# Kernel optimization log

Measured on AMD Instinct MI355X. Metric: run time of the kernel, lower is better.

## Reference

```python
import jax, jax.numpy as jnp
import numpy as np

B, C, H, W = 8, 512, 32, 32
NUM_HEADS = 8
HEAD_DIM = C // NUM_HEADS


def setup_inputs() -> dict:
    key = jax.random.key(0)
    k1, k2, k3 = jax.random.split(key, 3)
    query = jax.random.normal(k1, (B, C, H, W), dtype=jnp.float32)
    key_value = jax.random.normal(k2, (B, C, H, W), dtype=jnp.float32)
    # Linear(dim, 3*dim): store as [C, 3C] so y = x @ W + b
    W_qkv = jax.random.normal(k3, (C, 3 * C), dtype=jnp.float32) * (C ** -0.5)
    b_qkv = jnp.zeros((3 * C,), dtype=jnp.float32)
    return {"query": query, "key_value": key_value, "W_qkv": W_qkv, "b_qkv": b_qkv}


def reference(query, key_value, W_qkv, b_qkv):
    Bb, Cc, Hh, Ww = query.shape
    seq = Hh * Ww
    scale = HEAD_DIM ** -0.5

    # [B, C, H, W] -> [B, S, C]
    q_seq = query.reshape(Bb, Cc, seq).transpose(0, 2, 1)
    kv_seq = key_value.reshape(Bb, Cc, seq).transpose(0, 2, 1)

    # Original calls full qkv_proj and slices; math == projecting with sliced weights.
    q = q_seq @ W_qkv[:, :Cc] + b_qkv[:Cc]
    k = kv_seq @ W_qkv[:, Cc:2 * Cc] + b_qkv[Cc:2 * Cc]
    v = kv_seq @ W_qkv[:, 2 * Cc:] + b_qkv[2 * Cc:]

    def heads(x):  # [B, S, C] -> [B, nH, S, hd]
        return x.reshape(Bb, seq, NUM_HEADS, HEAD_DIM).transpose(0, 2, 1, 3)

    q, k, v = heads(q), heads(k), heads(v)
    attn = jnp.einsum('bhqd,bhkd->bhqk', q, k) * scale
    attn = jax.nn.softmax(attn, axis=-1)  # dropout: identity in eval
    out = jnp.einsum('bhqk,bhkd->bhqd', attn, v)
    # [B, nH, S, hd] -> [B, S, C] -> [B, C, H, W]
    out = out.transpose(0, 2, 1, 3).reshape(Bb, seq, Cc)
    return out.transpose(0, 2, 1).reshape(Bb, Cc, Hh, Ww)
```

## Files before the change

### kernel.cpp

```cpp
#include <hip/hip_runtime.h>
#include <hip/hip_bf16.h>

using short4v = __attribute__((ext_vector_type(4))) short;
using short8  = __attribute__((ext_vector_type(8))) short;
using uint2v  = __attribute__((ext_vector_type(2))) unsigned int;
using f32x4   = __attribute__((ext_vector_type(4))) float;

static constexpr int CDIM = 512;
static constexpr float KSCALE = 0.125f * 1.44269504088896341f;

__device__ __forceinline__ short f2bf(float f) {
  unsigned u = __builtin_bit_cast(unsigned, f);
  u = (u + 0x7fffu + ((u >> 16) & 1u)) >> 16;
  return (short)(unsigned short)u;
}

#define GLOAD_LDS16(gp, lp)                                                              \
  __builtin_amdgcn_global_load_lds((const __attribute__((address_space(1))) void*)(gp),  \
                                   (__attribute__((address_space(3))) void*)(lp), 16, 0, 0)
#define MFMA16(a, b, c) __builtin_amdgcn_mfma_f32_16x16x32_bf16((a), (b), (c), 0, 0, 0)

#define LDS_FENCE()                        \
  do {                                     \
    asm volatile("" ::: "memory");         \
    __builtin_amdgcn_s_waitcnt(0xc07f);    \
    __builtin_amdgcn_sched_barrier(0);     \
  } while (0)

#define TILE_SYNC(N)                                          \
  do {                                                        \
    __builtin_amdgcn_sched_barrier(0);                        \
    asm volatile("s_waitcnt vmcnt(" #N ")" ::: "memory");     \
    __builtin_amdgcn_sched_barrier(0);                        \
    __builtin_amdgcn_s_barrier();                             \
    asm volatile("" ::: "memory");                            \
    __builtin_amdgcn_sched_barrier(0);                        \
  } while (0)

#define TILE_BAR()                                            \
  do {                                                        \
    __builtin_amdgcn_sched_barrier(0);                        \
    asm volatile("s_waitcnt lgkmcnt(0)" ::: "memory");        \
    __builtin_amdgcn_sched_barrier(0);                        \
    __builtin_amdgcn_s_barrier();                             \
    asm volatile("" ::: "memory");                            \
    __builtin_amdgcn_sched_barrier(0);                        \
  } while (0)

__global__ __launch_bounds__(256) void prep_transpose(const float* __restrict__ query,
                                                      const float* __restrict__ keyv,
                                                      const float* __restrict__ Wqkv,
                                                      short* __restrict__ Xq_t,
                                                      short* __restrict__ Xkv_t,
                                                      short* __restrict__ W_t) {
  __shared__ float tile[64 * 65];
  const int id = blockIdx.x;
  const float* s; short* d; int R, C, r0, c0;
  if (id < 2048) {
    const int which = id >> 10;
    int rem = id & 1023;
    const int b = rem >> 7; rem &= 127;
    R = 512; C = 1024;
    s = (which ? keyv : query) + (size_t)b * 512 * 1024;
    d = (which ? Xkv_t : Xq_t) + (size_t)b * 512 * 1024;
    r0 = (rem >> 4) * 64; c0 = (rem & 15) * 64;
  } else {
    const int rem = id - 2048;
    R = 512; C = 1536; s = Wqkv; d = W_t;
    r0 = (rem / 24) * 64; c0 = (rem % 24) * 64;
  }
  const int t  = threadIdx.x;
  const int rr = t >> 4;
  const int c4 = (t & 15) * 4;
#pragma unroll
  for (int i = 0; i < 4; ++i) {
    const int r = rr + i * 16;
    f32x4 v = *(const f32x4*)(s + (size_t)(r0 + r) * C + c0 + c4);
#pragma unroll
    for (int j = 0; j < 4; ++j) tile[(c4 + j) * 65 + r] = v[j];
  }
  __syncthreads();
  const int r8 = (t & 7) * 8;
#pragma unroll
  for (int i = 0; i < 2; ++i) {
    const int c = (t >> 3) + i * 32;
    short8 pk;
#pragma unroll
    for (int j = 0; j < 8; ++j) pk[j] = f2bf(tile[c * 65 + r8 + j]);
    *(short8*)(d + (size_t)(c0 + c) * R + r0 + r8) = pk;
  }
}

__global__ __launch_bounds__(256, 3) void qkv_gemm(const short* __restrict__ Xq,
                                                   const short* __restrict__ Xkv,
                                                   const short* __restrict__ Wt,
                                                   const float* __restrict__ bias,
                                                   short* __restrict__ Qg,
                                                   short* __restrict__ Kg,
                                                   short* __restrict__ Vt) {
  __shared__ short Asm[128 * 64];
  __shared__ short Bsm[128 * 64];
  __shared__ short epi[4 * 1152];
  const int id = blockIdx.x;
  const int qq = id >> 3;
  const int m_blk = ((id & 7) << 3) | (qq & 7);
  const int n_blk = qq >> 3;
  const int m0 = m_blk << 7;
  const int n0 = n_blk << 7;
  const short* A = (n0 < CDIM) ? Xq : Xkv;
  const int t = threadIdx.x;
  const int w = t >> 6, l = t & 63;
  const int wm = w & 1, wn = w >> 1;
  const int lc = l & 15, lr = l >> 4;

  f32x4 acc[4][4];
#pragma unroll
  for (int i = 0; i < 4; ++i)
#pragma unroll
    for (int j = 0; j < 4; ++j) acc[i][j] = (f32x4){0.f, 0.f, 0.f, 0.f};

  for (int kb = 0; kb < 8; ++kb) {
    const int k0 = kb * 64;
#pragma unroll
    for (int i = 0; i < 4; ++i) {
      const int Qi = (w * 4 + i) * 64 + l;
      const int row = Qi >> 3, u = Qi & 7;
      GLOAD_LDS16(A + (size_t)(m0 + row) * CDIM + k0 + ((u ^ (row & 7)) * 8), &Asm[Qi * 8]);
      GLOAD_LDS16(Wt + (size_t)(n0 + row) * CDIM + k0 + ((u ^ (row & 7)) * 8), &Bsm[Qi * 8]);
    }
    __syncthreads();
#pragma unroll
    for (int kc = 0; kc < 2; ++kc) {
      short8 af[4], bfr[4];
#pragma unroll
      for (int mt = 0; mt < 4; ++mt) {
        const int row = wm * 64 + mt * 16 + lc;
        af[mt] = *(const short8*)(&Asm[(row * 8 + ((kc * 4 + lr) ^ (row & 7))) * 8]);
      }
#pragma unroll
      for (int nt = 0; nt < 4; ++nt) {
        const int row = wn * 64 + nt * 16 + lc;
        bfr[nt] = *(const short8*)(&Bsm[(row * 8 + ((kc * 4 + lr) ^ (row & 7))) * 8]);
      }
#pragma unroll
      for (int mt = 0; mt < 4; ++mt)
#pragma unroll
        for (int nt = 0; nt < 4; ++nt)
          acc[mt][nt] = MFMA16(af[mt], bfr[nt], acc[mt][nt]);
    }
    __syncthreads();
  }

  const int M0 = m0 + wm * 64;
  const int bb = M0 >> 10, s0 = M0 & 1023;
  const int N0 = n0 + wn * 64;
  float bv[4];
#pragma unroll
  for (int nt = 0; nt < 4; ++nt) bv[nt] = bias[N0 + nt * 16 + lc];
  short* slab = epi + w * 1152;

  const int hg = N0 >> 6;
  const int part = hg >> 3, hh = hg & 7;
  if (part < 2) {
    const float osc = part ? 1.f : KSCALE;
    short* obase = (part ? Kg : Qg) + (size_t)(bb * 8 + hh) * 65536 + (size_t)s0 * 64;
#pragma unroll
    for (int mt = 0; mt < 4; ++mt) {
#pragma unroll
      for (int ntL = 0; ntL < 4; ++ntL)
#pragma unroll
        for (int r = 0; r < 4; ++r)
          slab[(lr * 4 + r) * 72 + ntL * 16 + lc] =
              f2bf((acc[mt][ntL][r] + bv[ntL]) * osc);
      LDS_FENCE();
#pragma unroll
      for (int i = 0; i < 2; ++i) {
        const int slot = i * 64 + l;
        const int m_l = slot >> 3, n8 = (slot & 7) * 8;
        short8 vv = *(const short8*)(&slab[m_l * 72 + n8]);
        *(short8*)(obase + (size_t)(mt * 16 + m_l) * 64 + n8) = vv;
      }
      LDS_FENCE();
    }
  } else {
    short* vbase = Vt + (size_t)(bb * 8 + hh) * 65536;
#pragma unroll
    for (int ntL = 0; ntL < 4; ++ntL) {
#pragma unroll
      for (int mt = 0; mt < 4; ++mt)
#pragma unroll
        for (int r = 0; r < 4; ++r)
          slab[lc * 72 + mt * 16 + lr * 4 + r] = f2bf(acc[mt][ntL][r] + bv[ntL]);
      LDS_FENCE();
#pragma unroll
      for (int i = 0; i < 2; ++i) {
        const int slot = i * 64 + l;
        const int dloc = slot >> 3, ch = (slot & 7) * 8;
        short8 vv = *(const short8*)(&slab[dloc * 72 + ch]);
        *(short8*)(vbase + (size_t)(ntL * 16 + dloc) * 1024 + s0 + ch) = vv;
      }
      LDS_FENCE();
    }
  }
}

__global__ __launch_bounds__(256, 2) void flash_attn(const short* __restrict__ Qg,
                                                     const short* __restrict__ Kg,
                                                     const short* __restrict__ Vt,
                                                     float* __restrict__ out) {
  __shared__ alignas(16) short smem[25600];
  short* Ksm = smem;
  short* Vsm = smem + 8192;
  const int bh = blockIdx.x;
  const int b = bh >> 3, h = bh & 7;
  const int q0 = blockIdx.y * 128;
  const int t = threadIdx.x;
  const int w = t >> 6, l = t & 63;
  const int quad = l >> 4, l15 = l & 15;
  short* Pw = smem + 16384 + w * 2304;

  const short* Qbase = Qg + (size_t)bh * 65536;
  const short* Kbase = Kg + (size_t)bh * 65536;
  const short* Vbase = Vt + (size_t)bh * 65536;

  short8 bq[2][2];
#pragma unroll
  for (int qs = 0; qs < 2; ++qs) {
    const short* qrow = Qbase + (size_t)(q0 + qs * 64 + w * 16 + l15) * 64;
    bq[qs][0] = *(const short8*)(qrow + quad * 8);
    bq[qs][1] = *(const short8*)(qrow + 32 + quad * 8);
  }

  float lp[2] = {0.f, 0.f};
  f32x4 Oac[2][4];
#pragma unroll
  for (int qs = 0; qs < 2; ++qs)
#pragma unroll
    for (int dt = 0; dt < 4; ++dt) Oac[qs][dt] = (f32x4){0.f, 0.f, 0.f, 0.f};

  auto stage_tile = [&](int tile, int buf) {
    const int kk0 = tile * 64;
    short* Kd = Ksm + buf * 4096;
    short* Vd = Vsm + buf * 4096;
#pragma unroll
    for (int i = 0; i < 2; ++i) {
      const int Qi = (w * 2 + i) * 64 + l;
      const int sr = Qi >> 3, u = Qi & 7;
      GLOAD_LDS16(Kbase + (size_t)(kk0 + sr) * 64 + (u ^ (sr & 7)) * 8, &Kd[Qi * 8]);
      GLOAD_LDS16(Vbase + (size_t)sr * 1024 + kk0 + (u ^ (sr & 7)) * 8, &Vd[Qi * 8]);
    }
  };

  stage_tile(0, 0);
  for (int tt = 0; tt < 16; ++tt) {
    const int buf = tt & 1;
    if (tt < 15) {
      stage_tile(tt + 1, buf ^ 1);
      TILE_SYNC(4);
    } else {
      TILE_SYNC(0);
    }

    const short* Kh = Ksm + buf * 4096;
    const short* Vh = Vsm + buf * 4096;
    short8 kf[2][4];
#pragma unroll
    for (int c = 0; c < 2; ++c)
#pragma unroll
      for (int nt = 0; nt < 4; ++nt) {
        const int srow = nt * 16 + l15;
        kf[c][nt] = *(const short8*)(&Kh[(srow * 8 + ((c * 4 + quad) ^ (srow & 7))) * 8]);
      }

#pragma unroll
    for (int qs = 0; qs < 2; ++qs) {
      f32x4 st[4];
      __builtin_amdgcn_s_setprio(1);
#pragma unroll
      for (int nt = 0; nt < 4; ++nt) {
        st[nt] = (f32x4){0.f, 0.f, 0.f, 0.f};
#pragma unroll
        for (int c = 0; c < 2; ++c) st[nt] = MFMA16(kf[c][nt], bq[qs][c], st[nt]);
      }
      __builtin_amdgcn_s_setprio(0);
      short* Ps = Pw + qs * 1152;
#pragma unroll
      for (int nt = 0; nt < 4; ++nt) {
        float p0 = __builtin_amdgcn_exp2f(st[nt][0]);
        float p1 = __builtin_amdgcn_exp2f(st[nt][1]);
        float p2 = __builtin_amdgcn_exp2f(st[nt][2]);
        float p3 = __builtin_amdgcn_exp2f(st[nt][3]);
        lp[qs] += (p0 + p1) + (p2 + p3);
        unsigned pk0, pk1;
        asm("v_cvt_pk_bf16_f32 %0, %1, %2" : "=v"(pk0) : "v"(p0), "v"(p1));
        asm("v_cvt_pk_bf16_f32 %0, %1, %2" : "=v"(pk1) : "v"(p2), "v"(p3));
        uint2v pk; pk[0] = pk0; pk[1] = pk1;
        *(short4v*)(&Ps[l15 * 72 + (nt * 4 + quad) * 4]) = __builtin_bit_cast(short4v, pk);
      }
    }
    LDS_FENCE();

    __builtin_amdgcn_s_setprio(1);
#pragma unroll
    for (int c = 0; c < 2; ++c) {
      short8 pb0 = *(const short8*)(&Pw[l15 * 72 + (c * 8 + quad * 2) * 4]);
      short8 pb1 = *(const short8*)(&Pw[1152 + l15 * 72 + (c * 8 + quad * 2) * 4]);
#pragma unroll
      for (int dt = 0; dt < 4; ++dt) {
        const int drow = dt * 16 + l15;
        short8 vf = *(const short8*)(&Vh[(drow * 8 + ((c * 4 + quad) ^ (drow & 7))) * 8]);
        Oac[0][dt] = MFMA16(vf, pb0, Oac[0][dt]);
        Oac[1][dt] = MFMA16(vf, pb1, Oac[1][dt]);
      }
    }
    __builtin_amdgcn_s_setprio(0);
    TILE_BAR();
  }

#pragma unroll
  for (int qs = 0; qs < 2; ++qs) {
    float lv = lp[qs];
    lv += __shfl_xor(lv, 16, 64);
    lv += __shfl_xor(lv, 32, 64);
    const float rinv = 1.f / lv;
    float* ob = out + ((size_t)(b * 512 + h * 64)) * 1024 + q0 + qs * 64 + w * 16 + l15;
#pragma unroll
    for (int dt = 0; dt < 4; ++dt)
#pragma unroll
      for (int r = 0; r < 4; ++r)
        ob[(size_t)(dt * 16 + quad * 4 + r) * 1024] = Oac[qs][dt][r] * rinv;
  }
}

extern "C" void kernel_launch(void* const* d_in, const int* in_sizes, int n_in,
                              void* d_out, int out_size, void* d_ws, size_t ws_size,
                              hipStream_t stream) {
  const float* query = (const float*)d_in[0];
  const float* keyv  = (const float*)d_in[1];
  const float* Wqkv  = (const float*)d_in[2];
  const float* bqkv  = (const float*)d_in[3];
  float* out = (float*)d_out;
  short* ws  = (short*)d_ws;

  short* Xq_t  = ws;
  short* Xkv_t = ws + 4194304;
  short* W_t   = ws + 8388608;
  short* Qg    = ws + 9175040;
  short* Kg    = ws + 13369344;
  short* Vt    = ws + 17563648;

  prep_transpose<<<dim3(2240), 256, 0, stream>>>(query, keyv, Wqkv, Xq_t, Xkv_t, W_t);
  qkv_gemm<<<dim3(768), 256, 0, stream>>>(Xq_t, Xkv_t, W_t, bqkv, Qg, Kg, Vt);
  flash_attn<<<dim3(64, 8, 1), 256, 0, stream>>>(Qg, Kg, Vt, out);
}
```

Before: 127.2 us.

## Halve flash-attention query tile to 64 rows and swizzle P buffer in LDS

Each attention block now processes 64 query rows instead of 128, doubling the grid to 1024 blocks and raising the launch bound to 4 blocks per CU. Register and LDS use per block shrink, which allows more concurrent waves to hide latency. The per-wave P scratch drops its padded 72-stride layout for a 64-stride XOR-swizzled layout to avoid bank conflicts with less LDS. In exchange, each K/V tile is loaded from global memory twice as often relative to the compute done on it.

```diff
diff --git a/kernel.cpp b/kernel.cpp
--- a/kernel.cpp
+++ b/kernel.cpp
@@ -204,39 +204,36 @@
   }
 }
 
-__global__ __launch_bounds__(256, 2) void flash_attn(const short* __restrict__ Qg,
+__global__ __launch_bounds__(256, 4) void flash_attn(const short* __restrict__ Qg,
                                                      const short* __restrict__ Kg,
                                                      const short* __restrict__ Vt,
                                                      float* __restrict__ out) {
-  __shared__ alignas(16) short smem[25600];
+  __shared__ alignas(16) short smem[20480];
   short* Ksm = smem;
   short* Vsm = smem + 8192;
   const int bh = blockIdx.x;
   const int b = bh >> 3, h = bh & 7;
-  const int q0 = blockIdx.y * 128;
+  const int q0 = blockIdx.y * 64;
   const int t = threadIdx.x;
   const int w = t >> 6, l = t & 63;
   const int quad = l >> 4, l15 = l & 15;
-  short* Pw = smem + 16384 + w * 2304;
+  short* Pw = smem + 16384 + w * 1024;
 
   const short* Qbase = Qg + (size_t)bh * 65536;
   const short* Kbase = Kg + (size_t)bh * 65536;
   const short* Vbase = Vt + (size_t)bh * 65536;
 
-  short8 bq[2][2];
-#pragma unroll
-  for (int qs = 0; qs < 2; ++qs) {
-    const short* qrow = Qbase + (size_t)(q0 + qs * 64 + w * 16 + l15) * 64;
-    bq[qs][0] = *(const short8*)(qrow + quad * 8);
-    bq[qs][1] = *(const short8*)(qrow + 32 + quad * 8);
-  }
-
-  float lp[2] = {0.f, 0.f};
-  f32x4 Oac[2][4];
-#pragma unroll
-  for (int qs = 0; qs < 2; ++qs)
-#pragma unroll
-    for (int dt = 0; dt < 4; ++dt) Oac[qs][dt] = (f32x4){0.f, 0.f, 0.f, 0.f};
+  short8 bq[2];
+  {
+    const short* qrow = Qbase + (size_t)(q0 + w * 16 + l15) * 64;
+    bq[0] = *(const short8*)(qrow + quad * 8);
+    bq[1] = *(const short8*)(qrow + 32 + quad * 8);
+  }
+
+  float lp = 0.f;
+  f32x4 Oac[4];
+#pragma unroll
+  for (int dt = 0; dt < 4; ++dt) Oac[dt] = (f32x4){0.f, 0.f, 0.f, 0.f};
 
   auto stage_tile = [&](int tile, int buf) {
     const int kk0 = tile * 64;
@@ -272,64 +269,59 @@
         kf[c][nt] = *(const short8*)(&Kh[(srow * 8 + ((c * 4 + quad) ^ (srow & 7))) * 8]);
       }
 
-#pragma unroll
-    for (int qs = 0; qs < 2; ++qs) {
-      f32x4 st[4];
-      __builtin_amdgcn_s_setprio(1);
-#pragma unroll
-      for (int nt = 0; nt < 4; ++nt) {
-        st[nt] = (f32x4){0.f, 0.f, 0.f, 0.f};
-#pragma unroll
-        for (int c = 0; c < 2; ++c) st[nt] = MFMA16(kf[c][nt], bq[qs][c], st[nt]);
-      }
-      __builtin_amdgcn_s_setprio(0);
-      short* Ps = Pw + qs * 1152;
-#pragma unroll
-      for (int nt = 0; nt < 4; ++nt) {
-        float p0 = __builtin_amdgcn_exp2f(st[nt][0]);
-        float p1 = __builtin_amdgcn_exp2f(st[nt][1]);
-        float p2 = __builtin_amdgcn_exp2f(st[nt][2]);
-        float p3 = __builtin_amdgcn_exp2f(st[nt][3]);
-        lp[qs] += (p0 + p1) + (p2 + p3);
-        unsigned pk0, pk1;
-        asm("v_cvt_pk_bf16_f32 %0, %1, %2" : "=v"(pk0) : "v"(p0), "v"(p1));
-        asm("v_cvt_pk_bf16_f32 %0, %1, %2" : "=v"(pk1) : "v"(p2), "v"(p3));
-        uint2v pk; pk[0] = pk0; pk[1] = pk1;
-        *(short4v*)(&Ps[l15 * 72 + (nt * 4 + quad) * 4]) = __builtin_bit_cast(short4v, pk);
-      }
+    f32x4 st[4];
+    __builtin_amdgcn_s_setprio(1);
+#pragma unroll
+    for (int nt = 0; nt < 4; ++nt) {
+      st[nt] = (f32x4){0.f, 0.f, 0.f, 0.f};
+#pragma unroll
+      for (int c = 0; c < 2; ++c) st[nt] = MFMA16(kf[c][nt], bq[c], st[nt]);
+    }
+    __builtin_amdgcn_s_setprio(0);
+#pragma unroll
+    for (int nt = 0; nt < 4; ++nt) {
+      float p0 = __builtin_amdgcn_exp2f(st[nt][0]);
+      float p1 = __builtin_amdgcn_exp2f(st[nt][1]);
+      float p2 = __builtin_amdgcn_exp2f(st[nt][2]);
+      float p3 = __builtin_amdgcn_exp2f(st[nt][3]);
+      lp += (p0 + p1) + (p2 + p3);
+      unsigned pk0, pk1;
+      asm("v_cvt_pk_bf16_f32 %0, %1, %2" : "=v"(pk0) : "v"(p0), "v"(p1));
+      asm("v_cvt_pk_bf16_f32 %0, %1, %2" : "=v"(pk1) : "v"(p2), "v"(p3));
+      uint2v pk; pk[0] = pk0; pk[1] = pk1;
+      const int chunk = nt * 2 + (quad >> 1);
+      const int half  = quad & 1;
+      *(short4v*)(&Pw[l15 * 64 + ((chunk ^ (l15 & 7)) << 3) + (half << 2)]) =
+          __builtin_bit_cast(short4v, pk);
     }
     LDS_FENCE();
 
     __builtin_amdgcn_s_setprio(1);
 #pragma unroll
     for (int c = 0; c < 2; ++c) {
-      short8 pb0 = *(const short8*)(&Pw[l15 * 72 + (c * 8 + quad * 2) * 4]);
-      short8 pb1 = *(const short8*)(&Pw[1152 + l15 * 72 + (c * 8 + quad * 2) * 4]);
+      const int j = c * 4 + quad;
+      short8 pb = *(const short8*)(&Pw[l15 * 64 + ((j ^ (l15 & 7)) << 3)]);
 #pragma unroll
       for (int dt = 0; dt < 4; ++dt) {
         const int drow = dt * 16 + l15;
         short8 vf = *(const short8*)(&Vh[(drow * 8 + ((c * 4 + quad) ^ (drow & 7))) * 8]);
-        Oac[0][dt] = MFMA16(vf, pb0, Oac[0][dt]);
-        Oac[1][dt] = MFMA16(vf, pb1, Oac[1][dt]);
+        Oac[dt] = MFMA16(vf, pb, Oac[dt]);
       }
     }
     __builtin_amdgcn_s_setprio(0);
     TILE_BAR();
   }
 
-#pragma unroll
-  for (int qs = 0; qs < 2; ++qs) {
-    float lv = lp[qs];
-    lv += __shfl_xor(lv, 16, 64);
-    lv += __shfl_xor(lv, 32, 64);
-    const float rinv = 1.f / lv;
-    float* ob = out + ((size_t)(b * 512 + h * 64)) * 1024 + q0 + qs * 64 + w * 16 + l15;
-#pragma unroll
-    for (int dt = 0; dt < 4; ++dt)
-#pragma unroll
-      for (int r = 0; r < 4; ++r)
-        ob[(size_t)(dt * 16 + quad * 4 + r) * 1024] = Oac[qs][dt][r] * rinv;
-  }
+  float lv = lp;
+  lv += __shfl_xor(lv, 16, 64);
+  lv += __shfl_xor(lv, 32, 64);
+  const float rinv = 1.f / lv;
+  float* ob = out + ((size_t)(b * 512 + h * 64)) * 1024 + q0 + w * 16 + l15;
+#pragma unroll
+  for (int dt = 0; dt < 4; ++dt)
+#pragma unroll
+    for (int r = 0; r < 4; ++r)
+      ob[(size_t)(dt * 16 + quad * 4 + r) * 1024] = Oac[dt][r] * rinv;
 }
 
 extern "C" void kernel_launch(void* const* d_in, const int* in_sizes, int n_in,
@@ -351,5 +343,5 @@
 
   prep_transpose<<<dim3(2240), 256, 0, stream>>>(query, keyv, Wqkv, Xq_t, Xkv_t, W_t);
   qkv_gemm<<<dim3(768), 256, 0, stream>>>(Xq_t, Xkv_t, W_t, bqkv, Qg, Kg, Vt);
-  flash_attn<<<dim3(64, 8, 1), 256, 0, stream>>>(Qg, Kg, Vt, out);
-}
+  flash_attn<<<dim3(64, 16, 1), 256, 0, stream>>>(Qg, Kg, Vt, out);
+}
```

Measured after the change: 130.9 us. 1.03x slower.

## Replace double-buffered 64-key tiles with single-buffered 128-key chunks

Applied to the files above, without the earlier changes.

The attention loop no longer double-buffers 64-key K/V tiles. Each of 8 iterations now loads a 128-key chunk into one buffer, waits for it, and processes it as two 64-key halves, with a reworked swizzle for the wider V tile. This halves the number of barriers, but global loads no longer overlap compute, so every chunk exposes its load latency. The intent is to cut synchronisation overhead, relying on other resident workgroups to hide memory latency.

```diff
diff --git a/kernel.cpp b/kernel.cpp
--- a/kernel.cpp
+++ b/kernel.cpp
@@ -238,82 +238,75 @@
 #pragma unroll
     for (int dt = 0; dt < 4; ++dt) Oac[qs][dt] = (f32x4){0.f, 0.f, 0.f, 0.f};
 
-  auto stage_tile = [&](int tile, int buf) {
-    const int kk0 = tile * 64;
-    short* Kd = Ksm + buf * 4096;
-    short* Vd = Vsm + buf * 4096;
-#pragma unroll
-    for (int i = 0; i < 2; ++i) {
-      const int Qi = (w * 2 + i) * 64 + l;
+  for (int ch = 0; ch < 8; ++ch) {
+    const int kk0 = ch * 128;
+#pragma unroll
+    for (int i = 0; i < 4; ++i) {
+      const int Qi = i * 256 + t;
       const int sr = Qi >> 3, u = Qi & 7;
-      GLOAD_LDS16(Kbase + (size_t)(kk0 + sr) * 64 + (u ^ (sr & 7)) * 8, &Kd[Qi * 8]);
-      GLOAD_LDS16(Vbase + (size_t)sr * 1024 + kk0 + (u ^ (sr & 7)) * 8, &Vd[Qi * 8]);
-    }
-  };
-
-  stage_tile(0, 0);
-  for (int tt = 0; tt < 16; ++tt) {
-    const int buf = tt & 1;
-    if (tt < 15) {
-      stage_tile(tt + 1, buf ^ 1);
-      TILE_SYNC(4);
-    } else {
-      TILE_SYNC(0);
-    }
-
-    const short* Kh = Ksm + buf * 4096;
-    const short* Vh = Vsm + buf * 4096;
-    short8 kf[2][4];
-#pragma unroll
-    for (int c = 0; c < 2; ++c)
-#pragma unroll
-      for (int nt = 0; nt < 4; ++nt) {
-        const int srow = nt * 16 + l15;
-        kf[c][nt] = *(const short8*)(&Kh[(srow * 8 + ((c * 4 + quad) ^ (srow & 7))) * 8]);
-      }
-
-#pragma unroll
-    for (int qs = 0; qs < 2; ++qs) {
-      f32x4 st[4];
+      GLOAD_LDS16(Kbase + (size_t)(kk0 + sr) * 64 + ((u ^ (sr & 7)) * 8), &Ksm[Qi * 8]);
+      const int dv = Qi >> 4, uv = Qi & 15;
+      GLOAD_LDS16(Vbase + (size_t)dv * 1024 + kk0 + (((uv & 8) | ((uv & 7) ^ (dv & 7))) * 8),
+                  &Vsm[Qi * 8]);
+    }
+    TILE_SYNC(0);
+
+#pragma unroll
+    for (int half = 0; half < 2; ++half) {
+      short8 kf[2][4];
+#pragma unroll
+      for (int c = 0; c < 2; ++c)
+#pragma unroll
+        for (int nt = 0; nt < 4; ++nt) {
+          const int srow = half * 64 + nt * 16 + l15;
+          kf[c][nt] = *(const short8*)(&Ksm[(srow * 8 + ((c * 4 + quad) ^ (srow & 7))) * 8]);
+        }
+
+#pragma unroll
+      for (int qs = 0; qs < 2; ++qs) {
+        f32x4 st[4];
+        __builtin_amdgcn_s_setprio(1);
+#pragma unroll
+        for (int nt = 0; nt < 4; ++nt) {
+          st[nt] = (f32x4){0.f, 0.f, 0.f, 0.f};
+#pragma unroll
+          for (int c = 0; c < 2; ++c) st[nt] = MFMA16(kf[c][nt], bq[qs][c], st[nt]);
+        }
+        __builtin_amdgcn_s_setprio(0);
+        short* Ps = Pw + qs * 1152;
+#pragma unroll
+        for (int nt = 0; nt < 4; ++nt) {
+          float p0 = __builtin_amdgcn_exp2f(st[nt][0]);
+          float p1 = __builtin_amdgcn_exp2f(st[nt][1]);
+          float p2 = __builtin_amdgcn_exp2f(st[nt][2]);
+          float p3 = __builtin_amdgcn_exp2f(st[nt][3]);
+          lp[qs] += (p0 + p1) + (p2 + p3);
+          unsigned pk0, pk1;
+          asm("v_cvt_pk_bf16_f32 %0, %1, %2" : "=v"(pk0) : "v"(p0), "v"(p1));
+          asm("v_cvt_pk_bf16_f32 %0, %1, %2" : "=v"(pk1) : "v"(p2), "v"(p3));
+          uint2v pk; pk[0] = pk0; pk[1] = pk1;
+          *(short4v*)(&Ps[l15 * 72 + (nt * 4 + quad) * 4]) = __builtin_bit_cast(short4v, pk);
+        }
+      }
+      LDS_FENCE();
+
       __builtin_amdgcn_s_setprio(1);
 #pragma unroll
-      for (int nt = 0; nt < 4; ++nt) {
-        st[nt] = (f32x4){0.f, 0.f, 0.f, 0.f};
-#pragma unroll
-        for (int c = 0; c < 2; ++c) st[nt] = MFMA16(kf[c][nt], bq[qs][c], st[nt]);
+      for (int c = 0; c < 2; ++c) {
+        short8 pb0 = *(const short8*)(&Pw[l15 * 72 + (c * 8 + quad * 2) * 4]);
+        short8 pb1 = *(const short8*)(&Pw[1152 + l15 * 72 + (c * 8 + quad * 2) * 4]);
+#pragma unroll
+        for (int dt = 0; dt < 4; ++dt) {
+          const int drow = dt * 16 + l15;
+          short8 vf = *(const short8*)(
+              &Vsm[(drow * 16 + (half * 8 + ((c * 4 + quad) ^ (drow & 7)))) * 8]);
+          Oac[0][dt] = MFMA16(vf, pb0, Oac[0][dt]);
+          Oac[1][dt] = MFMA16(vf, pb1, Oac[1][dt]);
+        }
       }
       __builtin_amdgcn_s_setprio(0);
-      short* Ps = Pw + qs * 1152;
-#pragma unroll
-      for (int nt = 0; nt < 4; ++nt) {
-        float p0 = __builtin_amdgcn_exp2f(st[nt][0]);
-        float p1 = __builtin_amdgcn_exp2f(st[nt][1]);
-        float p2 = __builtin_amdgcn_exp2f(st[nt][2]);
-        float p3 = __builtin_amdgcn_exp2f(st[nt][3]);
-        lp[qs] += (p0 + p1) + (p2 + p3);
-        unsigned pk0, pk1;
-        asm("v_cvt_pk_bf16_f32 %0, %1, %2" : "=v"(pk0) : "v"(p0), "v"(p1));
-        asm("v_cvt_pk_bf16_f32 %0, %1, %2" : "=v"(pk1) : "v"(p2), "v"(p3));
-        uint2v pk; pk[0] = pk0; pk[1] = pk1;
-        *(short4v*)(&Ps[l15 * 72 + (nt * 4 + quad) * 4]) = __builtin_bit_cast(short4v, pk);
-      }
-    }
-    LDS_FENCE();
-
-    __builtin_amdgcn_s_setprio(1);
-#pragma unroll
-    for (int c = 0; c < 2; ++c) {
-      short8 pb0 = *(const short8*)(&Pw[l15 * 72 + (c * 8 + quad * 2) * 4]);
-      short8 pb1 = *(const short8*)(&Pw[1152 + l15 * 72 + (c * 8 + quad * 2) * 4]);
-#pragma unroll
-      for (int dt = 0; dt < 4; ++dt) {
-        const int drow = dt * 16 + l15;
-        short8 vf = *(const short8*)(&Vh[(drow * 8 + ((c * 4 + quad) ^ (drow & 7))) * 8]);
-        Oac[0][dt] = MFMA16(vf, pb0, Oac[0][dt]);
-        Oac[1][dt] = MFMA16(vf, pb1, Oac[1][dt]);
-      }
-    }
-    __builtin_amdgcn_s_setprio(0);
+      LDS_FENCE();
+    }
     TILE_BAR();
   }
 
```

New measurement: 130.9 us. 2.9% more time.
